# Performance work log

Measured on AMD Instinct MI355X. Metric: run time of the kernel, lower is better.

## Reference

```python
import jax, jax.numpy as jnp
import numpy as np

N = 4096        # nodes
F_IN = 256      # in_features
F_OUT = 64      # out_features
H = 64          # lstm_out_features
MAX_DEG = 64    # max neighbor count == max packed seq length
ALPHA = 0.2     # leaky relu negative slope
NEG = -9e15


def setup_inputs() -> dict:
    key = jax.random.key(0)
    ks = jax.random.split(key, 8)
    h = jax.random.normal(ks[0], (N, F_IN), dtype=jnp.float32)
    # per-node neighbor counts in [1, MAX_DEG]
    seq_length = jax.random.randint(ks[1], (N,), 1, MAX_DEG + 1, dtype=jnp.int32)
    # adjacency with exactly seq_length[i] ones in row i
    r = jax.random.uniform(ks[2], (N, N))
    ranks = jnp.argsort(jnp.argsort(-r, axis=1), axis=1)
    adj = (ranks < seq_length[:, None]).astype(jnp.float32)
    # parameters (xavier-ish scale)
    W = jax.random.normal(ks[3], (F_IN, F_OUT), dtype=jnp.float32) * (2.0 / (F_IN + F_OUT)) ** 0.5
    a = jax.random.normal(ks[4], (2 * F_OUT, 1), dtype=jnp.float32) * 0.1
    # backward-direction LSTM weights (torch gate order i,f,g,o); forward dir is unused in output
    w_ih = jax.random.normal(ks[5], (4 * H, F_OUT), dtype=jnp.float32) * 0.1
    w_hh = jax.random.normal(ks[6], (4 * H, H), dtype=jnp.float32) * 0.1
    b_ih = jnp.zeros((4 * H,), dtype=jnp.float32)
    b_hh = jnp.zeros((4 * H,), dtype=jnp.float32)
    return {"h": h, "adj": adj, "seq_length": seq_length, "W": W, "a": a,
            "w_ih": w_ih, "w_hh": w_hh, "b_ih": b_ih, "b_hh": b_hh}


def reference(h, adj, seq_length, W, a, w_ih, w_hh, b_ih, b_hh):
    n = h.shape[0]
    Wh = h @ W                                   # [N, F_OUT]
    # e[i,j] = leakyrelu(a_left . Wh_i + a_right . Wh_j)  (same math as O(N^2) concat)
    a1, a2 = a[:F_OUT, 0], a[F_OUT:, 0]
    e = jax.nn.leaky_relu((Wh @ a1)[:, None] + (Wh @ a2)[None, :], negative_slope=ALPHA)
    att = jax.nn.softmax(jnp.where(adj > 0, e, NEG), axis=1)   # [N, N]
    Wh2 = att @ Wh                               # aggregated node features [N, F_OUT]
    # sort neighbors by descending attention; LSTM only reads the first seq_length[i] <= MAX_DEG
    order = jnp.argsort(-att, axis=1)[:, :MAX_DEG]            # [N, T]
    seq = Wh2[order]                              # [N, T, F_OUT]
    # backward LSTM direction == run forward over the length-reversed sequence
    t = jnp.arange(MAX_DEG)
    rev_idx = jnp.clip(seq_length[:, None] - 1 - t[None, :], 0)
    rev = jnp.take_along_axis(seq, rev_idx[:, :, None], axis=1)  # [N, T, F_OUT]
    mask = t[None, :] < seq_length[:, None]                       # [N, T]

    def cell(carry, xm):
        hs, cs = carry
        x, m = xm                                 # x: [N, F_OUT], m: [N]
        gates = x @ w_ih.T + hs @ w_hh.T + b_ih + b_hh
        i, f, g, o = jnp.split(gates, 4, axis=1)
        c_new = jax.nn.sigmoid(f) * cs + jax.nn.sigmoid(i) * jnp.tanh(g)
        h_new = jax.nn.sigmoid(o) * jnp.tanh(c_new)
        m = m[:, None]
        return (jnp.where(m, h_new, hs), jnp.where(m, c_new, cs)), None

    init = (jnp.zeros((n, H), Wh.dtype), jnp.zeros((n, H), Wh.dtype))
    xs = (jnp.swapaxes(rev, 0, 1), mask.T)        # time-major
    (hn, _), _ = jax.lax.scan(cell, init, xs)
    return hn                                     # [N, H]  == torch hn[-1] (backward dir)
```

## Files before the change

### kernel.cpp

```cpp
#include <hip/hip_runtime.h>
#include <hip/hip_bf16.h>
#include <math.h>

#define N_NODES 4096
#define F_INN   256
#define F_OUTT  64
#define HID     64
#define MAXDEG  64

typedef __attribute__((ext_vector_type(8))) short bf16x8;
typedef __attribute__((ext_vector_type(4))) float f32x4;

__device__ int    g_mode;
__device__ int    g_anyArr[64];
__device__ float  g_Wh [N_NODES * F_OUTT];
__device__ float  g_s1 [N_NODES];
__device__ float  g_s2 [N_NODES];
__device__ int    g_rev[N_NODES * MAXDEG];
__device__ int    g_perm[N_NODES];
__device__ float4 g_GX [N_NODES * F_OUTT];

__device__ __forceinline__ float bf2f(unsigned short u) {
  union { unsigned int i; float f; } v; v.i = ((unsigned int)u) << 16; return v.f;
}
__device__ __forceinline__ unsigned short f2bf(float f) {
  union { __hip_bfloat16 b; unsigned short u; } v; v.b = __float2bfloat16(f); return v.u;
}

__device__ __forceinline__ float bcastf(float v, int l) {
  return __int_as_float(__builtin_amdgcn_readlane(__float_as_int(v), l));
}

__device__ __forceinline__ float rcp_fast(float x) { return __builtin_amdgcn_rcpf(x); }

__device__ __forceinline__ float sigm(float x) {
  return rcp_fast(1.f + __expf(-x));
}
__device__ __forceinline__ float tanh_fast(float x) {
  return fmaf(-2.f, rcp_fast(1.f + __expf(2.f * x)), 1.f);
}

__device__ __forceinline__ bf16x8 zfrag() {
  bf16x8 z;
  #pragma unroll
  for (int i = 0; i < 8; i++) z[i] = 0;
  return z;
}

__device__ __forceinline__ void block_sync_lds() {
  __asm__ volatile("s_waitcnt lgkmcnt(0)" ::: "memory");
  __builtin_amdgcn_s_barrier();
}

#define MFMA16(a, b, c) __builtin_amdgcn_mfma_f32_16x16x32_bf16((a), (b), (c), 0, 0, 0)

__global__ __launch_bounds__(256) void k_detect(const unsigned int* __restrict__ aw) {
  __shared__ int any;
  if (threadIdx.x == 0) any = 0;
  __syncthreads();
  const uint4 v = ((const uint4*)aw)[blockIdx.x * 256 + threadIdx.x];
  int loc = (int)((v.x & 0xFFFFu) | (v.y & 0xFFFFu) | (v.z & 0xFFFFu) | (v.w & 0xFFFFu));
  if (loc) atomicOr(&any, 1);
  __syncthreads();
  if (threadIdx.x == 0) g_anyArr[blockIdx.x] = any;
}

__global__ __launch_bounds__(256) void k_sort(const int* __restrict__ seq) {
  __shared__ int hist[MAXDEG + 1];
  __shared__ int offs[MAXDEG + 1];
  const int tid = threadIdx.x;
  if (tid <= MAXDEG) hist[tid] = 0;
  __syncthreads();
  if (tid == 0) {
    int any = 0;
    for (int b = 0; b < 64; b++) any |= g_anyArr[b];
    g_mode = any ? 1 : 0;
  }
  for (int i = tid; i < N_NODES; i += 256)
    atomicAdd(&hist[min(max(seq[i], 0), MAXDEG)], 1);
  __syncthreads();
  if (tid == 0) {
    int run = 0;
    for (int L = MAXDEG; L >= 0; L--) { offs[L] = run; run += hist[L]; }
  }
  __syncthreads();
  for (int i = tid; i < N_NODES; i += 256) {
    int p = atomicAdd(&offs[min(max(seq[i], 0), MAXDEG)], 1);
    g_perm[p] = i;
  }
}

__global__ __launch_bounds__(256) void k_wh(
    const void* __restrict__ h, const void* __restrict__ W, const void* __restrict__ a)
{
  const bool bf16 = (g_mode == 1);
  __shared__ float Ws[F_INN * F_OUTT];
  const int tid = threadIdx.x;
  if (bf16) {
    const ushort4* Wu = (const ushort4*)W;
    for (int v = tid; v < F_INN * F_OUTT / 4; v += 256) {
      ushort4 u = Wu[v];
      ((float4*)Ws)[v] = make_float4(bf2f(u.x), bf2f(u.y), bf2f(u.z), bf2f(u.w));
    }
  } else {
    const float4* Wf = (const float4*)W;
    for (int v = tid; v < F_INN * F_OUTT / 4; v += 256) ((float4*)Ws)[v] = Wf[v];
  }
  __syncthreads();
  const int wave = tid >> 6, lane = tid & 63;
  const int row = blockIdx.x * 4 + wave;
  float hr0, hr1, hr2, hr3;
  if (bf16) {
    ushort4 v = ((const ushort4*)((const unsigned short*)h + row * F_INN))[lane];
    hr0 = bf2f(v.x); hr1 = bf2f(v.y); hr2 = bf2f(v.z); hr3 = bf2f(v.w);
  } else {
    float4 v = ((const float4*)((const float*)h + row * F_INN))[lane];
    hr0 = v.x; hr1 = v.y; hr2 = v.z; hr3 = v.w;
  }
  double acc = 0.0;
  #pragma unroll 8
  for (int l = 0; l < 64; l++) {
    float h0 = bcastf(hr0, l), h1 = bcastf(hr1, l);
    float h2 = bcastf(hr2, l), h3 = bcastf(hr3, l);
    acc += (double)h0 * (double)Ws[(l * 4 + 0) * F_OUTT + lane];
    acc += (double)h1 * (double)Ws[(l * 4 + 1) * F_OUTT + lane];
    acc += (double)h2 * (double)Ws[(l * 4 + 2) * F_OUTT + lane];
    acc += (double)h3 * (double)Ws[(l * 4 + 3) * F_OUTT + lane];
  }
  const float whv = (float)acc;
  g_Wh[row * F_OUTT + lane] = whv;
  float a1, a2;
  if (bf16) {
    a1 = bf2f(((const unsigned short*)a)[lane]);
    a2 = bf2f(((const unsigned short*)a)[F_OUTT + lane]);
  } else {
    a1 = ((const float*)a)[lane];
    a2 = ((const float*)a)[F_OUTT + lane];
  }
  double t1 = (double)whv * (double)a1;
  double t2 = (double)whv * (double)a2;
  #pragma unroll
  for (int off = 32; off > 0; off >>= 1) {
    t1 += __shfl_down(t1, off);
    t2 += __shfl_down(t2, off);
  }
  if (lane == 0) { g_s1[row] = (float)t1; g_s2[row] = (float)t2; }
}

__global__ __launch_bounds__(256) void k_att(
    const void* __restrict__ adj, const void* __restrict__ w_ih,
    const void* __restrict__ b_ih, const void* __restrict__ b_hh)
{
  const bool bf16 = (g_mode == 1);
  const int i = blockIdx.x, tid = threadIdx.x;
  __shared__ int    nbr[MAXDEG];
  __shared__ float  att_s[MAXDEG];
  __shared__ int    sorted_j[MAXDEG];
  __shared__ double part[4][F_OUTT];
  __shared__ float  wh2row[F_OUTT];
  __shared__ int    cnt;
  if (tid == 0) cnt = 0;
  __syncthreads();
  if (bf16) {
    const uint4* ar = (const uint4*)((const unsigned short*)adj + (size_t)i * N_NODES);
    for (int c = tid; c < N_NODES / 8; c += 256) {
      uint4 v = ar[c];
      unsigned int w[4] = {v.x, v.y, v.z, v.w};
      #pragma unroll
      for (int k = 0; k < 4; k++) {
        if (w[k] & 0x0000FFFFu) { int p = atomicAdd(&cnt, 1); if (p < MAXDEG) nbr[p] = c*8 + k*2; }
        if (w[k] & 0xFFFF0000u) { int p = atomicAdd(&cnt, 1); if (p < MAXDEG) nbr[p] = c*8 + k*2 + 1; }
      }
    }
  } else {
    const float4* ar = (const float4*)((const float*)adj + (size_t)i * N_NODES);
    for (int c = tid; c < N_NODES / 4; c += 256) {
      float4 v = ar[c];
      if (v.x != 0.0f) { int p = atomicAdd(&cnt, 1); if (p < MAXDEG) nbr[p] = c*4;     }
      if (v.y != 0.0f) { int p = atomicAdd(&cnt, 1); if (p < MAXDEG) nbr[p] = c*4 + 1; }
      if (v.z != 0.0f) { int p = atomicAdd(&cnt, 1); if (p < MAXDEG) nbr[p] = c*4 + 2; }
      if (v.w != 0.0f) { int p = atomicAdd(&cnt, 1); if (p < MAXDEG) nbr[p] = c*4 + 3; }
    }
  }
  __syncthreads();
  const int L = min(cnt, MAXDEG);
  float ef = -3.0e38f; int jn = 0x7fffffff;
  if (tid < L) {
    jn = nbr[tid];
    float s = g_s1[i] + g_s2[jn];
    ef = (s > 0.0f) ? s : 0.2f * s;
  }
  float af = 0.0f;
  if (tid < 64) {
    float m = ef;
    #pragma unroll
    for (int off = 32; off > 0; off >>= 1) m = fmaxf(m, __shfl_down(m, off));
    m = __shfl(m, 0);
    double p = (tid < L) ? exp((double)(ef - m)) : 0.0;
    double ssum = p;
    #pragma unroll
    for (int off = 32; off > 0; off >>= 1) ssum += __shfl_down(ssum, off);
    ssum = __shfl(ssum, 0);
    af = (float)(p / ssum);
    att_s[tid] = af;
  }
  __syncthreads();
  if (tid < L) {
    int rank = 0;
    for (int q = 0; q < L; q++) {
      float aq = att_s[q]; int jq = nbr[q];
      if (aq > af || (aq == af && jq < jn)) rank++;
    }
    sorted_j[rank] = jn;
  }
  {
    const int wave = tid >> 6, lane = tid & 63;
    double acc = 0.0;
    for (int q = wave; q < L; q += 4)
      acc += (double)att_s[q] * (double)g_Wh[(size_t)nbr[q] * F_OUTT + lane];
    part[wave][lane] = acc;
  }
  __syncthreads();
  if (tid < MAXDEG)
    g_rev[i * MAXDEG + tid] = (tid < L) ? sorted_j[L - 1 - tid] : 0;
  if (tid < 64)
    wh2row[tid] = (float)(part[0][tid] + part[1][tid] + part[2][tid] + part[3][tid]);
  __syncthreads();
  {
    double acc = 0.0;
    if (bf16) {
      const uint2* wrow = (const uint2*)((const unsigned short*)w_ih + (size_t)tid * F_OUTT);
      #pragma unroll
      for (int q = 0; q < 16; q++) {
        uint2 v = wrow[q];
        acc += (double)bf2f((unsigned short)(v.x & 0xFFFFu)) * (double)wh2row[q*4 + 0];
        acc += (double)bf2f((unsigned short)(v.x >> 16))     * (double)wh2row[q*4 + 1];
        acc += (double)bf2f((unsigned short)(v.y & 0xFFFFu)) * (double)wh2row[q*4 + 2];
        acc += (double)bf2f((unsigned short)(v.y >> 16))     * (double)wh2row[q*4 + 3];
      }
      acc += (double)(bf2f(((const unsigned short*)b_ih)[tid]) +
                      bf2f(((const unsigned short*)b_hh)[tid]));
    } else {
      const float4* wrow = (const float4*)((const float*)w_ih + (size_t)tid * F_OUTT);
      #pragma unroll
      for (int q = 0; q < 16; q++) {
        float4 v = wrow[q];
        acc += (double)v.x * (double)wh2row[q*4 + 0];
        acc += (double)v.y * (double)wh2row[q*4 + 1];
        acc += (double)v.z * (double)wh2row[q*4 + 2];
        acc += (double)v.w * (double)wh2row[q*4 + 3];
      }
      acc += (double)(((const float*)b_ih)[tid] + ((const float*)b_hh)[tid]);
    }
    ((float*)g_GX)[(i * F_OUTT + (tid & 63)) * 4 + (tid >> 6)] = (float)acc;
  }
}

__global__ __launch_bounds__(256, 1) void k_lstm_mfma(
    const void* __restrict__ w_hh, const int* __restrict__ seq,
    void* __restrict__ out)
{
  const bool bf16 = (g_mode == 1);
  __shared__ __align__(16) unsigned short lds_h[2][16 * 72];
  __shared__ int lds_idx[16][MAXDEG];
  const int tid = threadIdx.x;
  const int w = tid >> 6, lane = tid & 63;
  const int q = lane >> 4, c = lane & 15;
  const int rb = blockIdx.x * 16;

  for (int v = tid; v < 16 * MAXDEG; v += 256) {
    const int e = v >> 6, t0 = v & (MAXDEG - 1);
    const int row = g_perm[rb + e] & (N_NODES - 1);
    lds_idx[e][t0] = g_rev[row * MAXDEG + t0] & (N_NODES - 1);
  }

  const int Lmax = min(max(seq[g_perm[rb] & (N_NODES - 1)], 0), MAXDEG);
  int row_e[4], Ls_e[4];
  #pragma unroll
  for (int r = 0; r < 4; r++) {
    row_e[r] = g_perm[rb + q * 4 + r] & (N_NODES - 1);
    Ls_e[r]  = min(max(seq[row_e[r]], 0), MAXDEG);
  }
  const int d_unit = 16 * w + c;

  bf16x8 Bhi[4][2];
  #pragma unroll
  for (int g = 0; g < 4; g++) {
    const int col = 64 * g + d_unit;
    #pragma unroll
    for (int ch = 0; ch < 2; ch++) {
      if (bf16) {
        Bhi[g][ch] = *(const bf16x8*)((const unsigned short*)w_hh + (size_t)col * 64 + ch * 32 + q * 8);
      } else {
        const float* wp = (const float*)w_hh + (size_t)col * 64 + ch * 32 + q * 8;
        float4 va = *(const float4*)wp, vb = *(const float4*)(wp + 4);
        bf16x8 f;
        f[0] = (short)f2bf(va.x); f[1] = (short)f2bf(va.y);
        f[2] = (short)f2bf(va.z); f[3] = (short)f2bf(va.w);
        f[4] = (short)f2bf(vb.x); f[5] = (short)f2bf(vb.y);
        f[6] = (short)f2bf(vb.z); f[7] = (short)f2bf(vb.w);
        Bhi[g][ch] = f;
      }
    }
  }

  __syncthreads();

  float4 gxb[4][4];
  #pragma unroll
  for (int s = 0; s < 4; s++) {
    #pragma unroll
    for (int r = 0; r < 4; r++)
      gxb[s][r] = g_GX[lds_idx[q * 4 + r][s] * F_OUTT + d_unit];
  }
  int idx_cur[4];
  #pragma unroll
  for (int r = 0; r < 4; r++) idx_cur[r] = lds_idx[q * 4 + r][4];

  bf16x8 h0 = zfrag(), h1 = zfrag();
  float cst[4] = {0.f, 0.f, 0.f, 0.f}, hst[4] = {0.f, 0.f, 0.f, 0.f};
  const int Lr = (Lmax + 3) & ~3;

  for (int t = 0; t < Lr; t += 4) {
    #pragma unroll
    for (int j = 0; j < 4; j++) {
      const int tt = t + j;
      f32x4 acc[4];
      #pragma unroll
      for (int g = 0; g < 4; g++) {
        f32x4 a;
        a[0] = (g==0)?gxb[j][0].x:(g==1)?gxb[j][0].y:(g==2)?gxb[j][0].z:gxb[j][0].w;
        a[1] = (g==0)?gxb[j][1].x:(g==1)?gxb[j][1].y:(g==2)?gxb[j][1].z:gxb[j][1].w;
        a[2] = (g==0)?gxb[j][2].x:(g==1)?gxb[j][2].y:(g==2)?gxb[j][2].z:gxb[j][2].w;
        a[3] = (g==0)?gxb[j][3].x:(g==1)?gxb[j][3].y:(g==2)?gxb[j][3].z:gxb[j][3].w;
        a = MFMA16(h0, Bhi[g][0], a);
        a = MFMA16(h1, Bhi[g][1], a);
        acc[g] = a;
      }
      #pragma unroll
      for (int r = 0; r < 4; r++)
        gxb[j][r] = g_GX[idx_cur[r] * F_OUTT + d_unit];
      {
        const int nt = min(tt + 5, MAXDEG - 1);
        #pragma unroll
        for (int r = 0; r < 4; r++) idx_cur[r] = lds_idx[q * 4 + r][nt];
      }
      unsigned short* lh = lds_h[j & 1];
      #pragma unroll
      for (int r = 0; r < 4; r++) {
        float ig = sigm(acc[0][r]);
        float fg = sigm(acc[1][r]);
        float gg = tanh_fast(acc[2][r]);
        float og = sigm(acc[3][r]);
        float cn = fg * cst[r] + ig * gg;
        float hn = og * tanh_fast(cn);
        bool live = (tt < Ls_e[r]);
        cst[r] = live ? cn : cst[r];
        hst[r] = live ? hn : hst[r];
        lh[(q * 4 + r) * 72 + d_unit] = f2bf(hst[r]);
      }
      block_sync_lds();
      {
        const unsigned short* lr_ = lds_h[j & 1] + c * 72;
        h0 = *(const bf16x8*)(lr_ + 8 * q);
        h1 = *(const bf16x8*)(lr_ + 32 + 8 * q);
      }
    }
  }
  #pragma unroll
  for (int r = 0; r < 4; r++) {
    if (bf16) ((__hip_bfloat16*)out)[row_e[r] * HID + d_unit] = __float2bfloat16(hst[r]);
    else      ((float*)out)[row_e[r] * HID + d_unit] = hst[r];
  }
}

extern "C" void kernel_launch(void* const* d_in, const int* in_sizes, int n_in,
                              void* d_out, int out_size, void* d_ws, size_t ws_size,
                              hipStream_t stream) {
  (void)in_sizes; (void)n_in; (void)out_size; (void)d_ws; (void)ws_size;
  const void* h    = d_in[0];
  const void* adj  = d_in[1];
  const int*  seq  = (const int*)d_in[2];
  const void* W    = d_in[3];
  const void* a    = d_in[4];
  const void* w_ih = d_in[5];
  const void* w_hh = d_in[6];
  const void* b_ih = d_in[7];
  const void* b_hh = d_in[8];

  k_detect   <<<64,           256, 0, stream>>>((const unsigned int*)adj);
  k_sort     <<<1,            256, 0, stream>>>(seq);
  k_wh       <<<N_NODES / 4,  256, 0, stream>>>(h, W, a);
  k_att      <<<N_NODES,      256, 0, stream>>>(adj, w_ih, b_ih, b_hh);
  k_lstm_mfma<<<N_NODES / 16, 256, 0, stream>>>(w_hh, seq, d_out);
}
```

Baseline: 227.2 us.

## Process one node per wavefront in attention kernel with ballot-based compaction

Restructures the attention kernel so each 64-lane wavefront handles one node instead of a whole 256-thread block per node. Neighbor discovery now uses wave ballots and mbcnt prefix counts instead of LDS atomics, so neighbor order is deterministic and no block barriers are needed. Softmax, ranking, aggregation and the w_ih projection move from double to float with fast exp and reciprocal, and ranking uses shuffles. This cuts sync, atomic and FP64 cost, at the price of small numerical differences that could flip tie-breaks in the attention sort.

```diff
diff --git a/kernel.cpp b/kernel.cpp
--- a/kernel.cpp
+++ b/kernel.cpp
@@ -38,6 +38,11 @@
 }
 __device__ __forceinline__ float tanh_fast(float x) {
   return fmaf(-2.f, rcp_fast(1.f + __expf(2.f * x)), 1.f);
+}
+
+__device__ __forceinline__ int mbcnt64(unsigned long long m) {
+  return __builtin_amdgcn_mbcnt_hi((unsigned)(m >> 32),
+         __builtin_amdgcn_mbcnt_lo((unsigned)(m & 0xFFFFFFFFull), 0));
 }
 
 __device__ __forceinline__ bf16x8 zfrag() {
@@ -152,108 +157,148 @@
     const void* __restrict__ b_ih, const void* __restrict__ b_hh)
 {
   const bool bf16 = (g_mode == 1);
-  const int i = blockIdx.x, tid = threadIdx.x;
-  __shared__ int    nbr[MAXDEG];
-  __shared__ float  att_s[MAXDEG];
-  __shared__ int    sorted_j[MAXDEG];
-  __shared__ double part[4][F_OUTT];
-  __shared__ float  wh2row[F_OUTT];
-  __shared__ int    cnt;
-  if (tid == 0) cnt = 0;
-  __syncthreads();
+  const int wv = threadIdx.x >> 6, lane = threadIdx.x & 63;
+  const int i = blockIdx.x * 4 + wv;
+
+  __shared__ int   s_nbr[4][MAXDEG];
+  __shared__ float s_att[4][MAXDEG];
+  __shared__ int   s_srt[4][MAXDEG];
+  __shared__ float s_wh2[4][F_OUTT];
+  int*   nbr  = s_nbr[wv];
+  float* attp = s_att[wv];
+  int*   srt  = s_srt[wv];
+  float* wh2  = s_wh2[wv];
+
+  int base = 0;
   if (bf16) {
     const uint4* ar = (const uint4*)((const unsigned short*)adj + (size_t)i * N_NODES);
-    for (int c = tid; c < N_NODES / 8; c += 256) {
-      uint4 v = ar[c];
-      unsigned int w[4] = {v.x, v.y, v.z, v.w};
+    #pragma unroll
+    for (int it = 0; it < 8; it++) {
+      const uint4 v = ar[it * 64 + lane];
+      unsigned word[4] = {v.x, v.y, v.z, v.w};
+      bool nz[8];
       #pragma unroll
       for (int k = 0; k < 4; k++) {
-        if (w[k] & 0x0000FFFFu) { int p = atomicAdd(&cnt, 1); if (p < MAXDEG) nbr[p] = c*8 + k*2; }
-        if (w[k] & 0xFFFF0000u) { int p = atomicAdd(&cnt, 1); if (p < MAXDEG) nbr[p] = c*8 + k*2 + 1; }
-      }
+        nz[2 * k]     = (word[k] & 0x0000FFFFu) != 0u;
+        nz[2 * k + 1] = (word[k] & 0xFFFF0000u) != 0u;
+      }
+      int pre = 0, tot = 0;
+      #pragma unroll
+      for (int k = 0; k < 8; k++) {
+        unsigned long long bl = __ballot(nz[k]);
+        pre += mbcnt64(bl);
+        tot += __popcll(bl);
+      }
+      int loc = 0;
+      #pragma unroll
+      for (int k = 0; k < 8; k++) {
+        if (nz[k]) {
+          int p = base + pre + loc;
+          if (p < MAXDEG) nbr[p] = it * 512 + lane * 8 + k;
+          loc++;
+        }
+      }
+      base += tot;
     }
   } else {
     const float4* ar = (const float4*)((const float*)adj + (size_t)i * N_NODES);
-    for (int c = tid; c < N_NODES / 4; c += 256) {
-      float4 v = ar[c];
-      if (v.x != 0.0f) { int p = atomicAdd(&cnt, 1); if (p < MAXDEG) nbr[p] = c*4;     }
-      if (v.y != 0.0f) { int p = atomicAdd(&cnt, 1); if (p < MAXDEG) nbr[p] = c*4 + 1; }
-      if (v.z != 0.0f) { int p = atomicAdd(&cnt, 1); if (p < MAXDEG) nbr[p] = c*4 + 2; }
-      if (v.w != 0.0f) { int p = atomicAdd(&cnt, 1); if (p < MAXDEG) nbr[p] = c*4 + 3; }
-    }
-  }
-  __syncthreads();
-  const int L = min(cnt, MAXDEG);
-  float ef = -3.0e38f; int jn = 0x7fffffff;
-  if (tid < L) {
-    jn = nbr[tid];
-    float s = g_s1[i] + g_s2[jn];
-    ef = (s > 0.0f) ? s : 0.2f * s;
-  }
-  float af = 0.0f;
-  if (tid < 64) {
-    float m = ef;
-    #pragma unroll
-    for (int off = 32; off > 0; off >>= 1) m = fmaxf(m, __shfl_down(m, off));
-    m = __shfl(m, 0);
-    double p = (tid < L) ? exp((double)(ef - m)) : 0.0;
-    double ssum = p;
-    #pragma unroll
-    for (int off = 32; off > 0; off >>= 1) ssum += __shfl_down(ssum, off);
-    ssum = __shfl(ssum, 0);
-    af = (float)(p / ssum);
-    att_s[tid] = af;
-  }
-  __syncthreads();
-  if (tid < L) {
+    #pragma unroll
+    for (int it = 0; it < 16; it++) {
+      const float4 v = ar[it * 64 + lane];
+      bool nz[4] = {v.x != 0.0f, v.y != 0.0f, v.z != 0.0f, v.w != 0.0f};
+      int pre = 0, tot = 0;
+      #pragma unroll
+      for (int k = 0; k < 4; k++) {
+        unsigned long long bl = __ballot(nz[k]);
+        pre += mbcnt64(bl);
+        tot += __popcll(bl);
+      }
+      int loc = 0;
+      #pragma unroll
+      for (int k = 0; k < 4; k++) {
+        if (nz[k]) {
+          int p = base + pre + loc;
+          if (p < MAXDEG) nbr[p] = it * 256 + lane * 4 + k;
+          loc++;
+        }
+      }
+      base += tot;
+    }
+  }
+  const int L = min(base, MAXDEG);
+
+  const int   jn  = (lane < L) ? nbr[lane] : 0;
+  const float s2v = g_s2[jn];
+  {
+    float s = g_s1[i] + s2v;
+    float e = (s > 0.0f) ? s : 0.2f * s;
+    if (lane >= L) e = -3.0e38f;
+    float m = e;
+    #pragma unroll
+    for (int off = 32; off > 0; off >>= 1) m = fmaxf(m, __shfl_xor(m, off));
+    float p = (lane < L) ? __expf(e - m) : 0.0f;
+    float ssum = p;
+    #pragma unroll
+    for (int off = 32; off > 0; off >>= 1) ssum += __shfl_xor(ssum, off);
+    const float av = p * rcp_fast(ssum);
+    attp[lane] = av;
     int rank = 0;
-    for (int q = 0; q < L; q++) {
-      float aq = att_s[q]; int jq = nbr[q];
-      if (aq > af || (aq == af && jq < jn)) rank++;
-    }
-    sorted_j[rank] = jn;
-  }
-  {
-    const int wave = tid >> 6, lane = tid & 63;
-    double acc = 0.0;
-    for (int q = wave; q < L; q += 4)
-      acc += (double)att_s[q] * (double)g_Wh[(size_t)nbr[q] * F_OUTT + lane];
-    part[wave][lane] = acc;
-  }
-  __syncthreads();
-  if (tid < MAXDEG)
-    g_rev[i * MAXDEG + tid] = (tid < L) ? sorted_j[L - 1 - tid] : 0;
-  if (tid < 64)
-    wh2row[tid] = (float)(part[0][tid] + part[1][tid] + part[2][tid] + part[3][tid]);
-  __syncthreads();
-  {
-    double acc = 0.0;
-    if (bf16) {
-      const uint2* wrow = (const uint2*)((const unsigned short*)w_ih + (size_t)tid * F_OUTT);
-      #pragma unroll
-      for (int q = 0; q < 16; q++) {
-        uint2 v = wrow[q];
-        acc += (double)bf2f((unsigned short)(v.x & 0xFFFFu)) * (double)wh2row[q*4 + 0];
-        acc += (double)bf2f((unsigned short)(v.x >> 16))     * (double)wh2row[q*4 + 1];
-        acc += (double)bf2f((unsigned short)(v.y & 0xFFFFu)) * (double)wh2row[q*4 + 2];
-        acc += (double)bf2f((unsigned short)(v.y >> 16))     * (double)wh2row[q*4 + 3];
-      }
-      acc += (double)(bf2f(((const unsigned short*)b_ih)[tid]) +
-                      bf2f(((const unsigned short*)b_hh)[tid]));
-    } else {
-      const float4* wrow = (const float4*)((const float*)w_ih + (size_t)tid * F_OUTT);
-      #pragma unroll
-      for (int q = 0; q < 16; q++) {
-        float4 v = wrow[q];
-        acc += (double)v.x * (double)wh2row[q*4 + 0];
-        acc += (double)v.y * (double)wh2row[q*4 + 1];
-        acc += (double)v.z * (double)wh2row[q*4 + 2];
-        acc += (double)v.w * (double)wh2row[q*4 + 3];
-      }
-      acc += (double)(((const float*)b_ih)[tid] + ((const float*)b_hh)[tid]);
-    }
-    ((float*)g_GX)[(i * F_OUTT + (tid & 63)) * 4 + (tid >> 6)] = (float)acc;
-  }
+    for (int qq = 0; qq < L; qq++) {
+      float aq = __shfl(av, qq);
+      int   jq = __shfl(jn, qq);
+      rank += (aq > av || (aq == av && jq < jn)) ? 1 : 0;
+    }
+    if (lane < L) srt[rank] = jn;
+  }
+  g_rev[i * MAXDEG + lane] = (lane < L) ? srt[L - 1 - lane] : 0;
+
+  float a0 = 0.f, a1 = 0.f, a2 = 0.f, a3 = 0.f;
+  int q = 0;
+  for (; q + 4 <= L; q += 4) {
+    const int j0 = nbr[q], j1 = nbr[q + 1], j2 = nbr[q + 2], j3 = nbr[q + 3];
+    const float t0 = attp[q], t1 = attp[q + 1], t2 = attp[q + 2], t3 = attp[q + 3];
+    a0 = fmaf(t0, g_Wh[(size_t)j0 * F_OUTT + lane], a0);
+    a1 = fmaf(t1, g_Wh[(size_t)j1 * F_OUTT + lane], a1);
+    a2 = fmaf(t2, g_Wh[(size_t)j2 * F_OUTT + lane], a2);
+    a3 = fmaf(t3, g_Wh[(size_t)j3 * F_OUTT + lane], a3);
+  }
+  for (; q < L; q++) {
+    const int j0 = nbr[q];
+    a0 = fmaf(attp[q], g_Wh[(size_t)j0 * F_OUTT + lane], a0);
+  }
+  wh2[lane] = (a0 + a1) + (a2 + a3);
+
+  float gx[4] = {0.f, 0.f, 0.f, 0.f};
+  if (bf16) {
+    #pragma unroll
+    for (int g = 0; g < 4; g++) {
+      const unsigned short* wr = (const unsigned short*)w_ih + (size_t)(g * 64 + lane) * F_OUTT;
+      #pragma unroll
+      for (int ch = 0; ch < 8; ch++) {
+        bf16x8 vv = *(const bf16x8*)(wr + ch * 8);
+        #pragma unroll
+        for (int e2 = 0; e2 < 8; e2++)
+          gx[g] = fmaf(bf2f((unsigned short)vv[e2]), wh2[ch * 8 + e2], gx[g]);
+      }
+      gx[g] += bf2f(((const unsigned short*)b_ih)[g * 64 + lane]) +
+               bf2f(((const unsigned short*)b_hh)[g * 64 + lane]);
+    }
+  } else {
+    #pragma unroll
+    for (int g = 0; g < 4; g++) {
+      const float* wr = (const float*)w_ih + (size_t)(g * 64 + lane) * F_OUTT;
+      #pragma unroll
+      for (int ch = 0; ch < 16; ch++) {
+        float4 vv = *(const float4*)(wr + ch * 4);
+        gx[g] = fmaf(vv.x, wh2[ch * 4 + 0], gx[g]);
+        gx[g] = fmaf(vv.y, wh2[ch * 4 + 1], gx[g]);
+        gx[g] = fmaf(vv.z, wh2[ch * 4 + 2], gx[g]);
+        gx[g] = fmaf(vv.w, wh2[ch * 4 + 3], gx[g]);
+      }
+      gx[g] += ((const float*)b_ih)[g * 64 + lane] + ((const float*)b_hh)[g * 64 + lane];
+    }
+  }
+  g_GX[(size_t)i * F_OUTT + lane] = make_float4(gx[0], gx[1], gx[2], gx[3]);
 }
 
 __global__ __launch_bounds__(256, 1) void k_lstm_mfma(
@@ -391,6 +436,6 @@
   k_detect   <<<64,           256, 0, stream>>>((const unsigned int*)adj);
   k_sort     <<<1,            256, 0, stream>>>(seq);
   k_wh       <<<N_NODES / 4,  256, 0, stream>>>(h, W, a);
-  k_att      <<<N_NODES,      256, 0, stream>>>(adj, w_ih, b_ih, b_hh);
+  k_att      <<<N_NODES / 4,  256, 0, stream>>>(adj, w_ih, b_ih, b_hh);
   k_lstm_mfma<<<N_NODES / 16, 256, 0, stream>>>(w_hh, seq, d_out);
 }
```

Result: slower. 233.5 us (+2.8%).
